# Kernel optimization log

Measured on AMD Instinct MI355X. Metric: run time of the kernel, lower is better.

The kernel has to match this reference:

```python
import jax, jax.numpy as jnp
import numpy as np

N = 50000      # nodes
E = 800000     # directed edges (before self-loops)
IN = 128       # in_channels
H = 4          # heads (layers 1,2)
C = 64         # hidden_channels per head
OUT = 512      # out_channels of final Linear
LEAKY_SLOPE = 0.2


def _gat_layer(x, src, dst, n, W, a_src, a_dst, b, concat):
    """PyG GATConv (v1): shared linear, additive attention, segment softmax over dst."""
    heads, ch = a_src.shape
    xl = (x @ W).reshape(n, heads, ch)                       # [N,H,C]
    as_n = jnp.sum(xl * a_src, axis=-1)                      # [N,H] alpha_src per node
    ad_n = jnp.sum(xl * a_dst, axis=-1)                      # [N,H] alpha_dst per node
    logits = jax.nn.leaky_relu(as_n[src] + ad_n[dst], LEAKY_SLOPE)  # [Etot,H]
    m = jax.lax.stop_gradient(jax.ops.segment_max(logits, dst, num_segments=n))
    p = jnp.exp(logits - m[dst])
    denom = jax.ops.segment_sum(p, dst, num_segments=n) + 1e-16
    alpha = p / denom[dst]                                   # segment softmax over incoming edges
    out = jax.ops.segment_sum(xl[src] * alpha[:, :, None], dst, num_segments=n)  # [N,H,C]
    out = out.reshape(n, heads * ch) if concat else out.mean(axis=1)
    return out + b


def setup_inputs() -> dict:
    key = jax.random.key(0)
    ks = jax.random.split(key, 16)

    def gl(k, shape, fan_in):
        return jax.random.normal(k, shape, dtype=jnp.float32) * np.float32(1.0 / np.sqrt(fan_in))

    x = jax.random.normal(ks[0], (N, IN), dtype=jnp.float32)
    edge_index = jax.random.randint(ks[1], (2, E), 0, N, dtype=jnp.int32)

    inp = {
        "x": x,
        "edge_index": edge_index,
        # layer 1: in -> H*C (concat)
        "W1": gl(ks[2], (IN, H * C), IN),
        "a_src1": gl(ks[3], (H, C), C),
        "a_dst1": gl(ks[4], (H, C), C),
        "b1": jnp.zeros((H * C,), jnp.float32),
        # layer 2: H*C -> H*C (concat)
        "W2": gl(ks[5], (H * C, H * C), H * C),
        "a_src2": gl(ks[6], (H, C), C),
        "a_dst2": gl(ks[7], (H, C), C),
        "b2": jnp.zeros((H * C,), jnp.float32),
        # layer 3: H*C -> C (1 head, no concat)
        "W3": gl(ks[8], (H * C, C), H * C),
        "a_src3": gl(ks[9], (1, C), C),
        "a_dst3": gl(ks[10], (1, C), C),
        "b3": jnp.zeros((C,), jnp.float32),
        # final fc: C -> OUT
        "Wfc": gl(ks[11], (C, OUT), C),
        "bfc": jnp.zeros((OUT,), jnp.float32),
    }
    return inp


def reference(x, edge_index, W1, a_src1, a_dst1, b1, W2, a_src2, a_dst2, b2,
              W3, a_src3, a_dst3, b3, Wfc, bfc):
    n = x.shape[0]
    loop = jnp.arange(n, dtype=edge_index.dtype)             # PyG GATConv adds self-loops
    src = jnp.concatenate([edge_index[0], loop])
    dst = jnp.concatenate([edge_index[1], loop])

    h = jax.nn.relu(_gat_layer(x, src, dst, n, W1, a_src1, a_dst1, b1, True))
    h = jax.nn.relu(_gat_layer(h, src, dst, n, W2, a_src2, a_dst2, b2, True))
    h = jax.nn.relu(_gat_layer(h, src, dst, n, W3, a_src3, a_dst3, b3, False))
    return jax.nn.relu(h @ Wfc + bfc)                        # [N, OUT]
```

## Files before the change

### kernel.cpp

```cpp
#include <hip/hip_runtime.h>
#include <cstdint>
#include <cstddef>

typedef unsigned short ushort_t;
typedef __bf16 bf16x8 __attribute__((ext_vector_type(8)));
typedef float f32x4 __attribute__((ext_vector_type(4)));

__device__ __forceinline__ float b2f(ushort_t u) {
    return __uint_as_float(((unsigned int)u) << 16);
}
__device__ __forceinline__ ushort_t f2b(float f) {
    __bf16 h = (__bf16)f;
    return *(ushort_t*)&h;
}
__device__ __forceinline__ float lo16(unsigned int u) { return __uint_as_float(u << 16); }
__device__ __forceinline__ float hi16(unsigned int u) { return __uint_as_float(u & 0xffff0000u); }
__device__ __forceinline__ unsigned int pack2(float a, float b) {
    return ((unsigned int)f2b(b) << 16) | (unsigned int)f2b(a);
}

__device__ __forceinline__ void stage8(const float* __restrict__ g, ushort_t* s) {
    float4 f0 = *(const float4*)g;
    float4 f1 = *(const float4*)(g + 4);
    union { ushort_t u[8]; uint4 v; } t;
    t.u[0] = f2b(f0.x); t.u[1] = f2b(f0.y); t.u[2] = f2b(f0.z); t.u[3] = f2b(f0.w);
    t.u[4] = f2b(f1.x); t.u[5] = f2b(f1.y); t.u[6] = f2b(f1.z); t.u[7] = f2b(f1.w);
    *(uint4*)s = t.v;
}
__device__ __forceinline__ void stage8(const ushort_t* __restrict__ g, ushort_t* s) {
    *(float4*)s = *(const float4*)g;
}

__device__ __forceinline__ void tr_seg(int id, const float* __restrict__ W,
                                       ushort_t* __restrict__ WT, int K, int N2) {
    int n = id / K, k = id - n * K;
    WT[id] = f2b(W[k * N2 + n]);
}
__global__ __launch_bounds__(256) void transpose_all_kernel(const float* __restrict__ W1,
                                                            const float* __restrict__ W2,
                                                            const float* __restrict__ W3,
                                                            const float* __restrict__ Wfc,
                                                            ushort_t* __restrict__ W1T,
                                                            ushort_t* __restrict__ W2T,
                                                            ushort_t* __restrict__ W3T,
                                                            ushort_t* __restrict__ WfcT,
                                                            int* __restrict__ deg, int n) {
    int id = blockIdx.x * 256 + threadIdx.x;
    if (id < n) deg[id] = 0;
    if (id < 32768) { tr_seg(id, W1, W1T, 128, 256); return; }
    id -= 32768;
    if (id < 65536) { tr_seg(id, W2, W2T, 256, 256); return; }
    id -= 65536;
    if (id < 16384) { tr_seg(id, W3, W3T, 256, 64); return; }
    id -= 16384;
    if (id < 32768) { tr_seg(id, Wfc, WfcT, 64, 512); return; }
}

__global__ __launch_bounds__(256) void degree_kernel(const int* __restrict__ ei_dst,
                                                     int* __restrict__ deg, int E, int Etot) {
    int e = blockIdx.x * 256 + threadIdx.x;
    if (e >= Etot) return;
    int d = (e < E) ? ei_dst[e] : (e - E);
    atomicAdd(&deg[d], 1);
}

__global__ __launch_bounds__(256) void partial_sum_kernel(const int* __restrict__ deg,
                                                          int* __restrict__ bsum, int n) {
    __shared__ int ws[4];
    int t = threadIdx.x;
    int i = blockIdx.x * 256 + t;
    int v = (i < n) ? deg[i] : 0;
#pragma unroll
    for (int off = 32; off; off >>= 1) v += __shfl_xor(v, off, 64);
    if ((t & 63) == 0) ws[t >> 6] = v;
    __syncthreads();
    if (t == 0) bsum[blockIdx.x] = ws[0] + ws[1] + ws[2] + ws[3];
}

__global__ __launch_bounds__(256) void scan_bsum_kernel(const int* __restrict__ bsum,
                                                        int* __restrict__ boff,
                                                        int* __restrict__ rowoff,
                                                        int nblk, int n) {
    __shared__ int sm[256];
    int t = threadIdx.x;
    int v = (t < nblk) ? bsum[t] : 0;
    sm[t] = v;
    __syncthreads();
#pragma unroll
    for (int off = 1; off < 256; off <<= 1) {
        int u = (t >= off) ? sm[t - off] : 0;
        __syncthreads();
        sm[t] += u;
        __syncthreads();
    }
    if (t < nblk) boff[t] = sm[t] - v;
    if (t == 255) rowoff[n] = sm[255];
}

__global__ __launch_bounds__(256) void block_scan_kernel(const int* __restrict__ deg,
                                                         const int* __restrict__ boff,
                                                         int* __restrict__ rowoff,
                                                         int* __restrict__ cursor, int n) {
    __shared__ int sm[256];
    int t = threadIdx.x;
    int i = blockIdx.x * 256 + t;
    int v = (i < n) ? deg[i] : 0;
    sm[t] = v;
    __syncthreads();
#pragma unroll
    for (int off = 1; off < 256; off <<= 1) {
        int u = (t >= off) ? sm[t - off] : 0;
        __syncthreads();
        sm[t] += u;
        __syncthreads();
    }
    if (i < n) {
        int r = boff[blockIdx.x] + sm[t] - v;
        rowoff[i] = r;
        cursor[i] = r;
    }
}

__global__ __launch_bounds__(256) void scatter_kernel(const int* __restrict__ ei_src,
                                                      const int* __restrict__ ei_dst,
                                                      int* __restrict__ cursor,
                                                      int* __restrict__ ssrc, int E, int Etot) {
    int e = blockIdx.x * 256 + threadIdx.x;
    if (e >= Etot) return;
    int s, d;
    if (e < E) { s = ei_src[e]; d = ei_dst[e]; } else { s = d = e - E; }
    int pos = atomicAdd(&cursor[d], 1);
    ssrc[pos] = s;
}

template <typename TA, int EPI, bool SMAJ>
__global__ __launch_bounds__(256) void gemm128_mfma(const TA* __restrict__ A,
                                                    const ushort_t* __restrict__ WT,
                                                    float* __restrict__ C,
                                                    ushort_t* __restrict__ Cb,
                                                    const float* __restrict__ bias,
                                                    const float* __restrict__ a_src,
                                                    const float* __restrict__ a_dst,
                                                    float* __restrict__ as_n,
                                                    float* __restrict__ ad_n,
                                                    int M, int K, int N2) {
    __shared__ ushort_t sA[128 * 32];
    __shared__ ushort_t sB[128 * 32];
    const int tid = threadIdx.x;
    const int wv = tid >> 6, lane = tid & 63;
    const int wr = wv >> 1, wc = wv & 1;
    const int quad = lane >> 4, l16 = lane & 15;
    const int bm = blockIdx.x * 128, bn = blockIdx.y * 128;
    const int sr0 = tid >> 2, sc = (tid & 3) * 8;
    const int sr1 = sr0 + 64;
    f32x4 acc[4][4] = {};

    int ga0 = bm + sr0; ga0 = ga0 < M ? ga0 : M - 1;
    int ga1 = bm + sr1; ga1 = ga1 < M ? ga1 : M - 1;
    const TA* pa0 = A + (size_t)ga0 * K + sc;
    const TA* pa1 = A + (size_t)ga1 * K + sc;
    const ushort_t* pb0 = WT + (size_t)(bn + sr0) * K + sc;
    const ushort_t* pb1 = WT + (size_t)(bn + sr1) * K + sc;

    for (int k0 = 0; k0 < K; k0 += 32) {
        stage8(pa0 + k0, sA + sr0 * 32 + sc);
        stage8(pa1 + k0, sA + sr1 * 32 + sc);
        stage8(pb0 + k0, sB + sr0 * 32 + sc);
        stage8(pb1 + k0, sB + sr1 * 32 + sc);
        __syncthreads();

        bf16x8 af[4], bfr[4];
#pragma unroll
        for (int m = 0; m < 4; m++)
            af[m] = *(const bf16x8*)(sA + (wr * 64 + m * 16 + l16) * 32 + quad * 8);
#pragma unroll
        for (int n = 0; n < 4; n++)
            bfr[n] = *(const bf16x8*)(sB + (wc * 64 + n * 16 + l16) * 32 + quad * 8);
#pragma unroll
        for (int m = 0; m < 4; m++)
#pragma unroll
            for (int n = 0; n < 4; n++)
                acc[m][n] = __builtin_amdgcn_mfma_f32_16x16x32_bf16(af[m], bfr[n], acc[m][n], 0, 0, 0);
        __syncthreads();
    }

#pragma unroll
    for (int n = 0; n < 4; n++) {
        int col = bn + wc * 64 + n * 16 + l16;
        float bv = (EPI == 1) ? bias[col] : 0.f;
#pragma unroll
        for (int m = 0; m < 4; m++) {
#pragma unroll
            for (int r = 0; r < 4; r++) {
                int row = bm + wr * 64 + m * 16 + quad * 4 + r;
                if (row < M) {
                    float v = acc[m][n][r];
                    if (EPI == 1) {
                        v += bv;
                        v = v > 0.f ? v : 0.f;
                        C[(size_t)row * N2 + col] = v;
                    } else if (SMAJ) {
                        Cb[((size_t)(col >> 5) * M + row) * 32 + (col & 31)] = f2b(v);
                    } else {
                        Cb[(size_t)row * N2 + col] = f2b(v);
                    }
                }
            }
        }
    }

    if (EPI == 2) {
        const int head = blockIdx.y * 2 + wc;
        float asv[4], adv[4];
#pragma unroll
        for (int n = 0; n < 4; n++) {
            asv[n] = a_src[head * 64 + n * 16 + l16];
            adv[n] = a_dst[head * 64 + n * 16 + l16];
        }
        float ps[4][4] = {}, pd[4][4] = {};
#pragma unroll
        for (int n = 0; n < 4; n++)
#pragma unroll
            for (int m = 0; m < 4; m++)
#pragma unroll
                for (int r = 0; r < 4; r++) {
                    ps[m][r] += acc[m][n][r] * asv[n];
                    pd[m][r] += acc[m][n][r] * adv[n];
                }
#pragma unroll
        for (int off = 1; off < 16; off <<= 1)
#pragma unroll
            for (int m = 0; m < 4; m++)
#pragma unroll
                for (int r = 0; r < 4; r++) {
                    ps[m][r] += __shfl_xor(ps[m][r], off, 64);
                    pd[m][r] += __shfl_xor(pd[m][r], off, 64);
                }
        if (l16 == 0) {
#pragma unroll
            for (int m = 0; m < 4; m++)
#pragma unroll
                for (int r = 0; r < 4; r++) {
                    int row = bm + wr * 64 + m * 16 + quad * 4 + r;
                    if (row < M) {
                        as_n[row * 4 + head] = ps[m][r];
                        ad_n[row * 4 + head] = pd[m][r];
                    }
                }
        }
    }
}

__global__ __launch_bounds__(256) void gemm64_mfma(const ushort_t* __restrict__ A,
                                                   const ushort_t* __restrict__ WT,
                                                   ushort_t* __restrict__ Cb,
                                                   const float* __restrict__ a_src,
                                                   const float* __restrict__ a_dst,
                                                   float* __restrict__ as_n,
                                                   float* __restrict__ ad_n,
                                                   int M, int K, int N2) {
    __shared__ ushort_t sA[64 * 32];
    __shared__ ushort_t sB[64 * 32];
    const int tid = threadIdx.x;
    const int wv = tid >> 6, lane = tid & 63;
    const int quad = lane >> 4, l16 = lane & 15;
    const int bm = blockIdx.x * 64;
    const int srow = tid >> 2, skof = (tid & 3) * 8;
    f32x4 acc[4] = {};

    int gm = bm + srow;
    gm = gm < M ? gm : M - 1;
    const ushort_t* pa = A + (size_t)gm * K + skof;
    const ushort_t* pb = WT + (size_t)srow * K + skof;

    for (int k0 = 0; k0 < K; k0 += 32) {
        *(float4*)(sA + srow * 32 + skof) = *(const float4*)(pa + k0);
        *(float4*)(sB + srow * 32 + skof) = *(const float4*)(pb + k0);
        __syncthreads();

        bf16x8 af = *(const bf16x8*)(sA + (wv * 16 + l16) * 32 + quad * 8);
#pragma unroll
        for (int j = 0; j < 4; j++) {
            bf16x8 bf = *(const bf16x8*)(sB + (j * 16 + l16) * 32 + quad * 8);
            acc[j] = __builtin_amdgcn_mfma_f32_16x16x32_bf16(af, bf, acc[j], 0, 0, 0);
        }
        __syncthreads();
    }

#pragma unroll
    for (int j = 0; j < 4; j++) {
        int col = j * 16 + l16;
#pragma unroll
        for (int r = 0; r < 4; r++) {
            int row = bm + wv * 16 + quad * 4 + r;
            if (row < M) Cb[(size_t)row * N2 + col] = f2b(acc[j][r]);
        }
    }

    float asv[4], adv[4];
#pragma unroll
    for (int j = 0; j < 4; j++) {
        asv[j] = a_src[j * 16 + l16];
        adv[j] = a_dst[j * 16 + l16];
    }
    float ps[4] = {}, pd[4] = {};
#pragma unroll
    for (int j = 0; j < 4; j++)
#pragma unroll
        for (int r = 0; r < 4; r++) {
            ps[r] += acc[j][r] * asv[j];
            pd[r] += acc[j][r] * adv[j];
        }
#pragma unroll
    for (int off = 1; off < 16; off <<= 1)
#pragma unroll
        for (int r = 0; r < 4; r++) {
            ps[r] += __shfl_xor(ps[r], off, 64);
            pd[r] += __shfl_xor(pd[r], off, 64);
        }
    if (l16 == 0) {
#pragma unroll
        for (int r = 0; r < 4; r++) {
            int row = bm + wv * 16 + quad * 4 + r;
            if (row < M) {
                as_n[row] = ps[r];
                ad_n[row] = pd[r];
            }
        }
    }
}

__global__ __launch_bounds__(256) void aggregate256_slice_kernel(
    const ushort_t* __restrict__ xs, const float* __restrict__ as_n,
    const float* __restrict__ ad_n, const int* __restrict__ rowoff,
    const int* __restrict__ ssrc, const float* __restrict__ bias,
    ushort_t* __restrict__ hout, int N) {
    const int bid = blockIdx.x;
    const int slice = bid & 7;
    const int db = bid >> 3;
    const int tid = threadIdx.x;
    const int wv = tid >> 6, lane = tid & 63;
    const int half = lane >> 5, l32 = lane & 31;
    const int slot = l32 >> 2, sub = l32 & 3;
    const int dd = db * 8 + wv * 2 + half;
    if (dd >= N) return;
    const int h = slice >> 1;
    const int r0 = rowoff[dd], r1 = rowoff[dd + 1];
    const float adv = ad_n[dd * 4 + h];
    const uint4* xv = (const uint4*)xs;
    const size_t sbase = (size_t)slice * N;
    float a0 = 0, a1 = 0, a2 = 0, a3 = 0, a4 = 0, a5 = 0, a6 = 0, a7 = 0, den = 0;
    for (int i = r0 + slot; i < r1; i += 8) {
        int s = ssrc[i];
        float lg = as_n[s * 4 + h] + adv;
        lg = lg > 0.f ? lg : 0.2f * lg;
        float p = __expf(lg);
        uint4 u = xv[(sbase + s) * 4 + sub];
        den += p;
        a0 += p * lo16(u.x); a1 += p * hi16(u.x);
        a2 += p * lo16(u.y); a3 += p * hi16(u.y);
        a4 += p * lo16(u.z); a5 += p * hi16(u.z);
        a6 += p * lo16(u.w); a7 += p * hi16(u.w);
    }
#pragma unroll
    for (int off = 4; off < 32; off <<= 1) {
        a0 += __shfl_xor(a0, off, 64); a1 += __shfl_xor(a1, off, 64);
        a2 += __shfl_xor(a2, off, 64); a3 += __shfl_xor(a3, off, 64);
        a4 += __shfl_xor(a4, off, 64); a5 += __shfl_xor(a5, off, 64);
        a6 += __shfl_xor(a6, off, 64); a7 += __shfl_xor(a7, off, 64);
        den += __shfl_xor(den, off, 64);
    }
    if (slot == 0) {
        float di = 1.f / (den + 1e-16f);
        const float4* bp = (const float4*)(bias + slice * 32 + sub * 8);
        float4 b0 = bp[0], b1 = bp[1];
        float v0 = a0 * di + b0.x, v1 = a1 * di + b0.y;
        float v2 = a2 * di + b0.z, v3 = a3 * di + b0.w;
        float v4 = a4 * di + b1.x, v5 = a5 * di + b1.y;
        float v6 = a6 * di + b1.z, v7 = a7 * di + b1.w;
        v0 = v0 > 0.f ? v0 : 0.f; v1 = v1 > 0.f ? v1 : 0.f;
        v2 = v2 > 0.f ? v2 : 0.f; v3 = v3 > 0.f ? v3 : 0.f;
        v4 = v4 > 0.f ? v4 : 0.f; v5 = v5 > 0.f ? v5 : 0.f;
        v6 = v6 > 0.f ? v6 : 0.f; v7 = v7 > 0.f ? v7 : 0.f;
        uint4 o;
        o.x = pack2(v0, v1); o.y = pack2(v2, v3);
        o.z = pack2(v4, v5); o.w = pack2(v6, v7);
        ((uint4*)hout)[(size_t)dd * 32 + slice * 4 + sub] = o;
    }
}

__global__ __launch_bounds__(256) void aggregate64_kernel(const ushort_t* __restrict__ xl,
                                                          const float* __restrict__ as_n,
                                                          const float* __restrict__ ad_n,
                                                          const int* __restrict__ rowoff,
                                                          const int* __restrict__ ssrc,
                                                          const float* __restrict__ bias,
                                                          ushort_t* __restrict__ hout, int N) {
    const int tid = threadIdx.x;
    const int wv = tid >> 6, lane = tid & 63;
    const uint4* xv = (const uint4*)xl;
    const int grp = lane >> 3, l8 = lane & 7;
    const int dd = blockIdx.x * 32 + wv * 8 + grp;
    if (dd >= N) return;
    const int r0 = rowoff[dd], r1 = rowoff[dd + 1];
    const float adv = ad_n[dd];
    float a0 = 0, a1 = 0, a2 = 0, a3 = 0, a4 = 0, a5 = 0, a6 = 0, a7 = 0, den = 0;
    for (int i = r0; i < r1; i += 8) {
        int s[8];
        float g[8];
        uint4 u[8];
#pragma unroll
        for (int j = 0; j < 8; j++) {
            int t = i + j;
            s[j] = ssrc[t < r1 ? t : r0];
        }
#pragma unroll
        for (int j = 0; j < 8; j++) g[j] = as_n[s[j]];
#pragma unroll
        for (int j = 0; j < 8; j++) u[j] = xv[(size_t)s[j] * 8 + l8];
#pragma unroll
        for (int j = 0; j < 8; j++) {
            float lg = g[j] + adv;
            lg = lg > 0.f ? lg : 0.2f * lg;
            float p = (i + j < r1) ? __expf(lg) : 0.f;
            den += p;
            a0 += p * lo16(u[j].x); a1 += p * hi16(u[j].x);
            a2 += p * lo16(u[j].y); a3 += p * hi16(u[j].y);
            a4 += p * lo16(u[j].z); a5 += p * hi16(u[j].z);
            a6 += p * lo16(u[j].w); a7 += p * hi16(u[j].w);
        }
    }
    float di = 1.f / (den + 1e-16f);
    float4 b0 = ((const float4*)bias)[l8 * 2];
    float4 b1 = ((const float4*)bias)[l8 * 2 + 1];
    float v0 = a0 * di + b0.x, v1 = a1 * di + b0.y;
    float v2 = a2 * di + b0.z, v3 = a3 * di + b0.w;
    float v4 = a4 * di + b1.x, v5 = a5 * di + b1.y;
    float v6 = a6 * di + b1.z, v7 = a7 * di + b1.w;
    v0 = v0 > 0.f ? v0 : 0.f; v1 = v1 > 0.f ? v1 : 0.f;
    v2 = v2 > 0.f ? v2 : 0.f; v3 = v3 > 0.f ? v3 : 0.f;
    v4 = v4 > 0.f ? v4 : 0.f; v5 = v5 > 0.f ? v5 : 0.f;
    v6 = v6 > 0.f ? v6 : 0.f; v7 = v7 > 0.f ? v7 : 0.f;
    uint4 o;
    o.x = pack2(v0, v1); o.y = pack2(v2, v3);
    o.z = pack2(v4, v5); o.w = pack2(v6, v7);
    ((uint4*)hout)[(size_t)dd * 8 + l8] = o;
}

extern "C" void kernel_launch(void* const* d_in, const int* in_sizes, int n_in,
                              void* d_out, int out_size, void* d_ws, size_t ws_size,
                              hipStream_t stream) {
    const int N = in_sizes[0] / 128;
    const int E = in_sizes[1] / 2;
    const int Etot = E + N;

    const float* x = (const float*)d_in[0];
    const int* ei = (const int*)d_in[1];
    const int* ei_src = ei;
    const int* ei_dst = ei + E;
    float* out = (float*)d_out;

    const float* as1 = (const float*)d_in[3];
    const float* ad1 = (const float*)d_in[4];
    const float* b1  = (const float*)d_in[5];
    const float* as2 = (const float*)d_in[7];
    const float* ad2 = (const float*)d_in[8];
    const float* b2  = (const float*)d_in[9];
    const float* as3 = (const float*)d_in[11];
    const float* ad3 = (const float*)d_in[12];
    const float* b3  = (const float*)d_in[13];
    const float* bfc = (const float*)d_in[15];

    ushort_t* bufX = (ushort_t*)d_ws;
    ushort_t* bufH = bufX + (size_t)N * 256;
    ushort_t* W1T  = bufH + (size_t)N * 256;
    ushort_t* W2T  = W1T + 32768;
    ushort_t* W3T  = W2T + 65536;
    ushort_t* WfcT = W3T + 16384;
    float* asn = (float*)(WfcT + 32768);
    float* adn = asn + (size_t)N * 4;
    int* deg    = (int*)(adn + (size_t)N * 4);
    int* rowoff = deg + N;
    int* cursor = rowoff + N + 1;
    int* ssrc   = cursor + N;
    int* bsum   = ssrc + Etot;
    int* boff   = bsum + 256;

    transpose_all_kernel<<<576, 256, 0, stream>>>((const float*)d_in[2], (const float*)d_in[6],
                                                  (const float*)d_in[10], (const float*)d_in[14],
                                                  W1T, W2T, W3T, WfcT, deg, N);

    int eb = (Etot + 255) / 256;
    degree_kernel<<<eb, 256, 0, stream>>>(ei_dst, deg, E, Etot);
    const int NBLK = (N + 255) / 256;
    partial_sum_kernel<<<NBLK, 256, 0, stream>>>(deg, bsum, N);
    scan_bsum_kernel<<<1, 256, 0, stream>>>(bsum, boff, rowoff, NBLK, N);
    block_scan_kernel<<<NBLK, 256, 0, stream>>>(deg, boff, rowoff, cursor, N);
    scatter_kernel<<<eb, 256, 0, stream>>>(ei_src, ei_dst, cursor, ssrc, E, Etot);

    const int MB128 = (N + 127) / 128;
    const int MB64 = (N + 63) / 64;
    const int nbS = ((N + 7) / 8) * 8;
    int nb32 = (N + 31) / 32;

    gemm128_mfma<float, 2, true><<<dim3(MB128, 2), 256, 0, stream>>>(
        x, W1T, nullptr, bufX, nullptr, as1, ad1, asn, adn, N, 128, 256);
    aggregate256_slice_kernel<<<nbS, 256, 0, stream>>>(bufX, asn, adn, rowoff, ssrc, b1, bufH, N);

    gemm128_mfma<ushort_t, 2, true><<<dim3(MB128, 2), 256, 0, stream>>>(
        bufH, W2T, nullptr, bufX, nullptr, as2, ad2, asn, adn, N, 256, 256);
    aggregate256_slice_kernel<<<nbS, 256, 0, stream>>>(bufX, asn, adn, rowoff, ssrc, b2, bufH, N);

    gemm64_mfma<<<dim3(MB64, 1), 256, 0, stream>>>(bufH, W3T, bufX, as3, ad3, asn, adn, N, 256, 64);
    aggregate64_kernel<<<nb32, 256, 0, stream>>>(bufX, asn, adn, rowoff, ssrc, b3, bufH, N);

    gemm128_mfma<ushort_t, 1, false><<<dim3(MB128, 4), 256, 0, stream>>>(
        bufH, WfcT, out, nullptr, bfc, nullptr, nullptr, nullptr, nullptr, N, 64, 512);
}
```

Before: 541.1 us.

## Give each 4-lane group a whole destination node with 8-way unrolled edge loads

The slice aggregation kernel now maps one destination node to each group of 4 lanes, so a wave covers 16 destinations and a block covers 64, instead of spreading 8 edge slots across 32 lanes per destination. Each group walks its own edge list in chunks of 8, issuing all index, logit and feature loads for a chunk before using them, and masks the tail with zero weights. This drops the cross-lane shuffle reduction and the idle slots on low-degree nodes, and adds memory-level parallelism within each thread. In exchange it costs more registers per thread, creates load imbalance between lanes whose nodes differ in degree, and wastes loads on the padded tail of each chunk.

```diff
diff --git a/kernel.cpp b/kernel.cpp
--- a/kernel.cpp
+++ b/kernel.cpp
@@ -340,9 +340,8 @@
     const int db = bid >> 3;
     const int tid = threadIdx.x;
     const int wv = tid >> 6, lane = tid & 63;
-    const int half = lane >> 5, l32 = lane & 31;
-    const int slot = l32 >> 2, sub = l32 & 3;
-    const int dd = db * 8 + wv * 2 + half;
+    const int grp = lane >> 2, sub = lane & 3;
+    const int dd = db * 64 + wv * 16 + grp;
     if (dd >= N) return;
     const int h = slice >> 1;
     const int r0 = rowoff[dd], r1 = rowoff[dd + 1];
@@ -350,43 +349,46 @@
     const uint4* xv = (const uint4*)xs;
     const size_t sbase = (size_t)slice * N;
     float a0 = 0, a1 = 0, a2 = 0, a3 = 0, a4 = 0, a5 = 0, a6 = 0, a7 = 0, den = 0;
-    for (int i = r0 + slot; i < r1; i += 8) {
-        int s = ssrc[i];
-        float lg = as_n[s * 4 + h] + adv;
-        lg = lg > 0.f ? lg : 0.2f * lg;
-        float p = __expf(lg);
-        uint4 u = xv[(sbase + s) * 4 + sub];
-        den += p;
-        a0 += p * lo16(u.x); a1 += p * hi16(u.x);
-        a2 += p * lo16(u.y); a3 += p * hi16(u.y);
-        a4 += p * lo16(u.z); a5 += p * hi16(u.z);
-        a6 += p * lo16(u.w); a7 += p * hi16(u.w);
-    }
-#pragma unroll
-    for (int off = 4; off < 32; off <<= 1) {
-        a0 += __shfl_xor(a0, off, 64); a1 += __shfl_xor(a1, off, 64);
-        a2 += __shfl_xor(a2, off, 64); a3 += __shfl_xor(a3, off, 64);
-        a4 += __shfl_xor(a4, off, 64); a5 += __shfl_xor(a5, off, 64);
-        a6 += __shfl_xor(a6, off, 64); a7 += __shfl_xor(a7, off, 64);
-        den += __shfl_xor(den, off, 64);
-    }
-    if (slot == 0) {
-        float di = 1.f / (den + 1e-16f);
-        const float4* bp = (const float4*)(bias + slice * 32 + sub * 8);
-        float4 b0 = bp[0], b1 = bp[1];
-        float v0 = a0 * di + b0.x, v1 = a1 * di + b0.y;
-        float v2 = a2 * di + b0.z, v3 = a3 * di + b0.w;
-        float v4 = a4 * di + b1.x, v5 = a5 * di + b1.y;
-        float v6 = a6 * di + b1.z, v7 = a7 * di + b1.w;
-        v0 = v0 > 0.f ? v0 : 0.f; v1 = v1 > 0.f ? v1 : 0.f;
-        v2 = v2 > 0.f ? v2 : 0.f; v3 = v3 > 0.f ? v3 : 0.f;
-        v4 = v4 > 0.f ? v4 : 0.f; v5 = v5 > 0.f ? v5 : 0.f;
-        v6 = v6 > 0.f ? v6 : 0.f; v7 = v7 > 0.f ? v7 : 0.f;
-        uint4 o;
-        o.x = pack2(v0, v1); o.y = pack2(v2, v3);
-        o.z = pack2(v4, v5); o.w = pack2(v6, v7);
-        ((uint4*)hout)[(size_t)dd * 32 + slice * 4 + sub] = o;
-    }
+    for (int i = r0; i < r1; i += 8) {
+        int s[8];
+        float g[8];
+        uint4 u[8];
+#pragma unroll
+        for (int j = 0; j < 8; j++) {
+            int t = i + j;
+            s[j] = ssrc[t < r1 ? t : r0];
+        }
+#pragma unroll
+        for (int j = 0; j < 8; j++) g[j] = as_n[s[j] * 4 + h];
+#pragma unroll
+        for (int j = 0; j < 8; j++) u[j] = xv[(sbase + s[j]) * 4 + sub];
+#pragma unroll
+        for (int j = 0; j < 8; j++) {
+            float lg = g[j] + adv;
+            lg = lg > 0.f ? lg : 0.2f * lg;
+            float p = (i + j < r1) ? __expf(lg) : 0.f;
+            den += p;
+            a0 += p * lo16(u[j].x); a1 += p * hi16(u[j].x);
+            a2 += p * lo16(u[j].y); a3 += p * hi16(u[j].y);
+            a4 += p * lo16(u[j].z); a5 += p * hi16(u[j].z);
+            a6 += p * lo16(u[j].w); a7 += p * hi16(u[j].w);
+        }
+    }
+    float di = 1.f / (den + 1e-16f);
+    const float4* bp = (const float4*)(bias + slice * 32 + sub * 8);
+    float4 b0 = bp[0], b1 = bp[1];
+    float v0 = a0 * di + b0.x, v1 = a1 * di + b0.y;
+    float v2 = a2 * di + b0.z, v3 = a3 * di + b0.w;
+    float v4 = a4 * di + b1.x, v5 = a5 * di + b1.y;
+    float v6 = a6 * di + b1.z, v7 = a7 * di + b1.w;
+    v0 = v0 > 0.f ? v0 : 0.f; v1 = v1 > 0.f ? v1 : 0.f;
+    v2 = v2 > 0.f ? v2 : 0.f; v3 = v3 > 0.f ? v3 : 0.f;
+    v4 = v4 > 0.f ? v4 : 0.f; v5 = v5 > 0.f ? v5 : 0.f;
+    v6 = v6 > 0.f ? v6 : 0.f; v7 = v7 > 0.f ? v7 : 0.f;
+    uint4 o;
+    o.x = pack2(v0, v1); o.y = pack2(v2, v3);
+    o.z = pack2(v4, v5); o.w = pack2(v6, v7);
+    ((uint4*)hout)[(size_t)dd * 32 + slice * 4 + sub] = o;
 }
 
 __global__ __launch_bounds__(256) void aggregate64_kernel(const ushort_t* __restrict__ xl,
@@ -500,7 +502,7 @@
 
     const int MB128 = (N + 127) / 128;
     const int MB64 = (N + 63) / 64;
-    const int nbS = ((N + 7) / 8) * 8;
+    const int nbS = ((N + 63) / 64) * 8;
     int nb32 = (N + 31) / 32;
 
     gemm128_mfma<float, 2, true><<<dim3(MB128, 2), 256, 0, stream>>>(
```

Result: faster. 516.4 us (-4.6%).
